# Kernel tuning notes

Measured on AMD Instinct MI355X. Metric: run time of the kernel, lower is better.

The kernel has to match this reference:

```python
import jax, jax.numpy as jnp
import numpy as np

DIM, E, K, H = 1024, 8, 2, 4096

def setup_inputs() -> dict:
    key = jax.random.key(0)
    ks = jax.random.split(key, 5)
    s_in = 1.0 / np.sqrt(DIM)
    s_h = 1.0 / np.sqrt(H)
    return {
        "x": jax.random.normal(ks[0], (4, 2048, DIM), dtype=jnp.float32),
        "Wr": jax.random.normal(ks[1], (DIM, E), dtype=jnp.float32) * s_in,
        "W1": jax.random.normal(ks[2], (E, DIM, H), dtype=jnp.float32) * s_in,
        "b1": jnp.zeros((E, H), dtype=jnp.float32),
        "W2": jax.random.normal(ks[3], (E, H, DIM), dtype=jnp.float32) * s_h,
        "b2": jnp.zeros((E, DIM), dtype=jnp.float32),
    }

def reference(x, Wr, W1, b1, W2, b2):
    batch, seq, dim = x.shape
    x_flat = x.reshape(-1, dim)                      # [T, D]
    logits = x_flat @ Wr                             # [T, E]
    w, ind = jax.lax.top_k(logits, K)                # [T, K]
    w = jax.nn.softmax(w, axis=-1)
    # combine[t, e] = sum_i w[t, i] * (ind[t, i] == e)
    combine = jnp.einsum('tke,tk->te', jax.nn.one_hot(ind, E, dtype=x.dtype), w)  # [T, E]

    def body(acc, params):
        W1e, b1e, W2e, b2e, ce = params
        h = jax.nn.gelu(x_flat @ W1e + b1e, approximate=False)  # exact GELU (torch nn.GELU default)
        y = h @ W2e + b2e                                        # [T, D]
        return acc + ce[:, None] * y, None

    out0 = jnp.zeros_like(x_flat)
    out, _ = jax.lax.scan(body, out0, (W1, b1, W2, b2, combine.T))
    return out.reshape(batch, seq, dim)
```

## Files before the change

### kernel.cpp

```cpp
#include <hip/hip_runtime.h>
#include <hip/hip_bf16.h>

#define TDIM 1024
#define NEXP 8
#define NHID 4096

typedef __hip_bfloat16 bf16;
typedef __attribute__((ext_vector_type(8))) short bf16x8;
typedef __attribute__((ext_vector_type(8))) unsigned short u16x8;
typedef __attribute__((ext_vector_type(4))) float f32x4;

__device__ __forceinline__ void gload_lds16(void* lds, const void* g) {
  __builtin_amdgcn_global_load_lds(
      (const __attribute__((address_space(1))) unsigned int*)g,
      (__attribute__((address_space(3))) unsigned int*)lds, 16, 0, 0);
}

__device__ __forceinline__ unsigned short f2bf_bits(float f) {
  __hip_bfloat16 b = __float2bfloat16(f);
  unsigned short u;
  __builtin_memcpy(&u, &b, 2);
  return u;
}

__device__ __forceinline__ float bf2f(unsigned short u) {
  union { unsigned int i; float f; } c;
  c.i = ((unsigned int)u) << 16;
  return c.f;
}

__global__ void cvt_x_kernel(const float* __restrict__ x, bf16* __restrict__ xb, int n4) {
  int i = blockIdx.x * blockDim.x + threadIdx.x;
  if (i >= n4) return;
  float4 v = reinterpret_cast<const float4*>(x)[i];
  ushort4 o;
  o.x = f2bf_bits(v.x);
  o.y = f2bf_bits(v.y);
  o.z = f2bf_bits(v.z);
  o.w = f2bf_bits(v.w);
  reinterpret_cast<ushort4*>(xb)[i] = o;
}

__global__ __launch_bounds__(256) void transpose_cvt_kernel(const float* __restrict__ in,
                                                            bf16* __restrict__ out, int R, int C) {
  __shared__ float tile[64][65];
  const size_t eoff = (size_t)blockIdx.z * R * C;
  const float* src = in + eoff;
  bf16* dst = out + eoff;
  const int c0 = blockIdx.x * 64, r0 = blockIdx.y * 64;
  const int tid = threadIdx.x;
#pragma unroll
  for (int i = 0; i < 4; ++i) {
    int s = tid + i * 256;
    int r = s >> 4, cg = (s & 15) * 4;
    float4 v = *reinterpret_cast<const float4*>(src + (size_t)(r0 + r) * C + c0 + cg);
    tile[r][cg] = v.x;
    tile[r][cg + 1] = v.y;
    tile[r][cg + 2] = v.z;
    tile[r][cg + 3] = v.w;
  }
  __syncthreads();
#pragma unroll
  for (int i = 0; i < 2; ++i) {
    int s = tid + i * 256;
    int c = s >> 3, rg = (s & 7) * 8;
    u16x8 o;
#pragma unroll
    for (int j = 0; j < 8; ++j) o[j] = f2bf_bits(tile[rg + j][c]);
    *reinterpret_cast<u16x8*>(dst + (size_t)(c0 + c) * R + r0 + rg) = o;
  }
}

__global__ void router_kernel(const float* __restrict__ x, const float* __restrict__ Wr,
                              int* __restrict__ idx, float* __restrict__ wtok,
                              int* __restrict__ cnt, int T) {
  int wave = (blockIdx.x * blockDim.x + threadIdx.x) >> 6;
  int lane = threadIdx.x & 63;
  if (wave >= T) return;
  const float4* xr4 = reinterpret_cast<const float4*>(x + (size_t)wave * TDIM);
  const float4* wr4 = reinterpret_cast<const float4*>(Wr);
  float acc[NEXP];
#pragma unroll
  for (int e = 0; e < NEXP; ++e) acc[e] = 0.f;
#pragma unroll
  for (int i = 0; i < TDIM / 256; ++i) {
    float4 xv = xr4[lane + i * 64];
    int row = (lane + i * 64) * 4;
#pragma unroll
    for (int j = 0; j < 4; ++j) {
      float xs = (&xv.x)[j];
      float4 wa = wr4[(row + j) * 2];
      float4 wb = wr4[(row + j) * 2 + 1];
      acc[0] += xs * wa.x;
      acc[1] += xs * wa.y;
      acc[2] += xs * wa.z;
      acc[3] += xs * wa.w;
      acc[4] += xs * wb.x;
      acc[5] += xs * wb.y;
      acc[6] += xs * wb.z;
      acc[7] += xs * wb.w;
    }
  }
#pragma unroll
  for (int e = 0; e < NEXP; ++e) {
    float v = acc[e];
#pragma unroll
    for (int s = 32; s; s >>= 1) v += __shfl_xor(v, s);
    acc[e] = v;
  }
  if (lane == 0) {
    int e0 = 0;
    float l0 = acc[0];
    for (int e = 1; e < NEXP; ++e)
      if (acc[e] > l0) { l0 = acc[e]; e0 = e; }
    int e1 = -1;
    float l1 = -INFINITY;
    for (int e = 0; e < NEXP; ++e)
      if (e != e0 && acc[e] > l1) { l1 = acc[e]; e1 = e; }
    float z = __expf(l1 - l0);
    float w0 = 1.f / (1.f + z);
    float w1 = z / (1.f + z);
    idx[wave * 2] = e0;
    idx[wave * 2 + 1] = e1;
    wtok[wave * 2] = w0;
    wtok[wave * 2 + 1] = w1;
    atomicAdd(&cnt[e0], 1);
    atomicAdd(&cnt[e1], 1);
  }
}

__global__ void scan_kernel(const int* __restrict__ cnt, int* __restrict__ offs) {
  if (threadIdx.x == 0 && blockIdx.x == 0) {
    int s = 0;
    for (int e = 0; e < NEXP; ++e) { offs[e] = s; s += cnt[e]; }
  }
}

__global__ void build_perm_kernel(const int* __restrict__ idx, const int* __restrict__ offs,
                                  int* __restrict__ fill, int* __restrict__ perm,
                                  int* __restrict__ islot, int T) {
  int t = blockIdx.x * blockDim.x + threadIdx.x;
  if (t >= T) return;
#pragma unroll
  for (int k = 0; k < 2; ++k) {
    int e = idx[t * 2 + k];
    int p = offs[e] + atomicAdd(&fill[e], 1);
    perm[p] = t;
    islot[t * 2 + k] = p;
  }
}

template <int KD, int ND, bool GATHER, bool GELU>
__global__ __launch_bounds__(512, 2) void moe_gemm8(
    const bf16* __restrict__ A, const bf16* __restrict__ BT, const float* __restrict__ bias,
    const int* __restrict__ perm, const int* __restrict__ cnt, const int* __restrict__ offs,
    bf16* __restrict__ Dst, int nm, int nn) {
  __shared__ short lds[65536];

  const int nwg = NEXP * nm * nn;
  const int bid = blockIdx.x;
  const int wg = (bid & 7) * (nwg >> 3) + (bid >> 3);
  const int e = wg / (nm * nn);
  const int rem = wg % (nm * nn);
  const int mb = rem / nn, nb = rem % nn;

  const int ce = cnt[e];
  const int m0 = mb * 256;
  if (m0 >= ce) return;
  const int base = offs[e];
  const int n0 = nb * 256;
  const int tid = threadIdx.x;
  const int lane = tid & 63;
  const int wid = tid >> 6;
  const int wm = wid >> 2, wn = wid & 3;
  const int lcol = lane & 15;
  const int lkg = (lane >> 4) * 8;

  const int kxs0 = ((lkg << 1) ^ ((lcol & 7) << 4)) >> 1;
  const int kxs1 = (((lkg + 32) << 1) ^ ((lcol & 7) << 4)) >> 1;
  int aRow[4], bRow[2];
#pragma unroll
  for (int mm = 0; mm < 4; ++mm) aRow[mm] = (wm * 64 + mm * 16 + lcol) << 6;
#pragma unroll
  for (int n2 = 0; n2 < 2; ++n2) bRow[n2] = (wn * 32 + n2 * 16 + lcol) << 6;

  const bf16* aP[2][2];
  const bf16* bP[2][2];
#pragma unroll
  for (int h = 0; h < 2; ++h)
#pragma unroll
    for (int i = 0; i < 2; ++i) {
      int s = tid + i * 512;
      int srow = s >> 3;
      int kof = ((s & 7) ^ (srow & 7)) * 8;
      int grow = m0 + h * 128 + srow;
      if (grow > ce - 1) grow = ce - 1;
      size_t arow = GATHER ? (size_t)perm[base + grow] : (size_t)(base + grow);
      aP[h][i] = A + arow * KD + kof;
      bP[h][i] = BT + ((size_t)e * ND + n0 + h * 128 + srow) * KD + kof;
    }

  f32x4 acc[8][4];
#pragma unroll
  for (int m = 0; m < 8; ++m)
#pragma unroll
    for (int n = 0; n < 4; ++n) acc[m][n] = (f32x4){0.f, 0.f, 0.f, 0.f};

#define STAGE(SBUF, OP, HF, kof)                                                     \
  {                                                                                  \
    char* sd = (char*)lds + (SBUF) * 65536 + (OP) * 32768 + (HF) * 16384 + tid * 16; \
    gload_lds16(sd, ((OP) ? bP[HF][0] : aP[HF][0]) + (kof));                         \
    gload_lds16(sd + 8192, ((OP) ? bP[HF][1] : aP[HF][1]) + (kof));                  \
  }

#define PHASE(p, CBUF, SBUF, kof, DO_VM)                                             \
  {                                                                                  \
    constexpr int OP = (p) & 1;                           \
    constexpr int HF = ((p) >> 1) & 1;                  \
    STAGE(SBUF, OP, HF, kof);                                                        \
    if (DO_VM) asm volatile("s_waitcnt vmcnt(6)" ::: "memory");                      \
    __builtin_amdgcn_s_barrier();                                                    \
    asm volatile("" ::: "memory");                                                   \
    const short* Ab = lds + (CBUF) * 32768 + OP * 8192;                              \
    const short* Bb = lds + (CBUF) * 32768 + 16384 + HF * 8192;                      \
    bf16x8 fA[4][2], fB[2][2];                                                       \
    _Pragma("unroll") for (int n2 = 0; n2 < 2; ++n2) {                               \
      fB[n2][0] = *(const bf16x8*)(Bb + bRow[n2] + kxs0);                            \
      fB[n2][1] = *(const bf16x8*)(Bb + bRow[n2] + kxs1);                            \
    }                                                                                \
    _Pragma("unroll") for (int mm = 0; mm < 4; ++mm) {                               \
      fA[mm][0] = *(const bf16x8*)(Ab + aRow[mm] + kxs0);                            \
      fA[mm][1] = *(const bf16x8*)(Ab + aRow[mm] + kxs1);                            \
    }                                                                                \
    asm volatile("s_waitcnt lgkmcnt(0)" ::: "memory");                               \
    __builtin_amdgcn_s_setprio(1);                                                   \
    _Pragma("unroll") for (int mm = 0; mm < 4; ++mm)                                 \
        _Pragma("unroll") for (int n2 = 0; n2 < 2; ++n2) {                           \
      acc[OP * 4 + mm][HF * 2 + n2] = __builtin_amdgcn_mfma_f32_16x16x32_bf16(       \
          fA[mm][0], fB[n2][0], acc[OP * 4 + mm][HF * 2 + n2], 0, 0, 0);             \
      acc[OP * 4 + mm][HF * 2 + n2] = __builtin_amdgcn_mfma_f32_16x16x32_bf16(       \
          fA[mm][1], fB[n2][1], acc[OP * 4 + mm][HF * 2 + n2], 0, 0, 0);             \
    }                                                                                \
    __builtin_amdgcn_s_setprio(0);                                                   \
  }

  STAGE(0, 0, 0, 0);
  STAGE(0, 1, 0, 0);
  STAGE(0, 0, 1, 0);
  STAGE(0, 1, 1, 0);

  const int NI = KD / 128;
  for (int itv = 0; itv < NI; ++itv) {
    const int k1 = itv * 128 + 64;
    int k2 = itv * 128 + 128;
    if (k2 >= KD) k2 = 0;
    PHASE(0, 0, 1, k1, 1)
    PHASE(1, 0, 1, k1, 1)
    PHASE(2, 0, 1, k1, 1)
    PHASE(3, 0, 1, k1, 0)
    PHASE(4, 1, 0, k2, 1)
    PHASE(5, 1, 0, k2, 1)
    PHASE(6, 1, 0, k2, 1)
    PHASE(7, 1, 0, k2, 0)
  }
#undef PHASE
#undef STAGE

  float bv[4];
#pragma unroll
  for (int ni = 0; ni < 4; ++ni)
    bv[ni] = bias[e * ND + n0 + (ni >> 1) * 128 + wn * 32 + (ni & 1) * 16 + lcol];
  const int lr4 = (lane >> 4) * 4;
#pragma unroll
  for (int mi = 0; mi < 8; ++mi) {
    const int rbase = m0 + (mi >> 2) * 128 + wm * 64 + (mi & 3) * 16 + lr4;
#pragma unroll
    for (int r = 0; r < 4; ++r) {
      int grow = rbase + r;
      if (grow < ce) {
        bf16* drow = Dst + (size_t)(base + grow) * ND;
#pragma unroll
        for (int ni = 0; ni < 4; ++ni) {
          int col = n0 + (ni >> 1) * 128 + wn * 32 + (ni & 1) * 16 + lcol;
          float v = acc[mi][ni][r] + bv[ni];
          if (GELU) v = 0.5f * v * (1.0f + erff(v * 0.70710678118654752f));
          drow[col] = __float2bfloat16(v);
        }
      }
    }
  }
}

__global__ void combine_kernel(const bf16* __restrict__ y, const int* __restrict__ islot,
                               const float* __restrict__ wtok, float* __restrict__ out) {
  const int t = blockIdx.x;
  const int d = threadIdx.x * 4;
  const int s0 = islot[t * 2], s1 = islot[t * 2 + 1];
  const float w0 = wtok[t * 2], w1 = wtok[t * 2 + 1];
  ushort4 ya = *reinterpret_cast<const ushort4*>(y + (size_t)s0 * TDIM + d);
  ushort4 yb = *reinterpret_cast<const ushort4*>(y + (size_t)s1 * TDIM + d);
  float4 o;
  o.x = w0 * bf2f(ya.x) + w1 * bf2f(yb.x);
  o.y = w0 * bf2f(ya.y) + w1 * bf2f(yb.y);
  o.z = w0 * bf2f(ya.z) + w1 * bf2f(yb.z);
  o.w = w0 * bf2f(ya.w) + w1 * bf2f(yb.w);
  *reinterpret_cast<float4*>(out + (size_t)t * TDIM + d) = o;
}

extern "C" void kernel_launch(void* const* d_in, const int* in_sizes, int n_in, void* d_out,
                              int out_size, void* d_ws, size_t ws_size, hipStream_t stream) {
  const float* x = (const float*)d_in[0];
  const float* Wr = (const float*)d_in[1];
  const float* W1 = (const float*)d_in[2];
  const float* b1 = (const float*)d_in[3];
  const float* W2 = (const float*)d_in[4];
  const float* b2 = (const float*)d_in[5];
  float* out = (float*)d_out;
  const int T = in_sizes[0] / TDIM;

  size_t off = 0;
  auto alloc = [&](size_t bytes) {
    void* q = (char*)d_ws + off;
    off += (bytes + 255) & ~(size_t)255;
    return q;
  };
  bf16* xb = (bf16*)alloc((size_t)T * TDIM * 2);
  bf16* W1T = (bf16*)alloc((size_t)NEXP * TDIM * NHID * 2);
  bf16* W2T = (bf16*)alloc((size_t)NEXP * TDIM * NHID * 2);
  bf16* h = (bf16*)alloc((size_t)2 * T * NHID * 2);
  int* idx = (int*)alloc((size_t)T * 2 * 4);
  float* wtok = (float*)alloc((size_t)T * 2 * 4);
  int* perm = (int*)alloc((size_t)T * 2 * 4);
  int* islot = (int*)alloc((size_t)T * 2 * 4);
  int* cnt = (int*)alloc(256);
  int* fill = cnt + 8;
  int* offs = cnt + 16;
  bf16* y = W1T;

  hipMemsetAsync(cnt, 0, 64, stream);

  cvt_x_kernel<<<(T * TDIM / 4 + 255) / 256, 256, 0, stream>>>(x, xb, T * TDIM / 4);
  transpose_cvt_kernel<<<dim3(NHID / 64, TDIM / 64, NEXP), 256, 0, stream>>>(W1, W1T, TDIM, NHID);
  transpose_cvt_kernel<<<dim3(TDIM / 64, NHID / 64, NEXP), 256, 0, stream>>>(W2, W2T, NHID, TDIM);
  router_kernel<<<T / 4, 256, 0, stream>>>(x, Wr, idx, wtok, cnt, T);
  scan_kernel<<<1, 64, 0, stream>>>(cnt, offs);
  build_perm_kernel<<<(T + 255) / 256, 256, 0, stream>>>(idx, offs, fill, perm, islot, T);

  moe_gemm8<TDIM, NHID, true, true><<<NEXP * 32 * 16, 512, 0, stream>>>(
      xb, W1T, b1, perm, cnt, offs, h, 32, 16);
  moe_gemm8<NHID, TDIM, false, false><<<NEXP * 32 * 4, 512, 0, stream>>>(
      h, W2T, b2, perm, cnt, offs, y, 32, 4);

  combine_kernel<<<T, 256, 0, stream>>>(y, islot, wtok, out);
}
```

Measured before the change: 826.7 us.

## Fuse prep kernels into one launch and reorder GEMM phases for fragment reuse

Merges the x conversion, both weight transpose-converts and the router into a single prep kernel, with the router wave also writing the bf16 copy of x so x is read once. Inside the MoE GEMM, the phase order is changed to a serpentine walk over the 2x2 quadrants so each phase reloads only the A or only the B fragments from LDS, keeping the other in registers. This cuts launch overhead, one pass over x, and half of the LDS fragment reads per phase, at the cost of longer live ranges for the fragment registers.

```diff
diff --git a/kernel.cpp b/kernel.cpp
--- a/kernel.cpp
+++ b/kernel.cpp
@@ -29,26 +29,10 @@
   return c.f;
 }
 
-__global__ void cvt_x_kernel(const float* __restrict__ x, bf16* __restrict__ xb, int n4) {
-  int i = blockIdx.x * blockDim.x + threadIdx.x;
-  if (i >= n4) return;
-  float4 v = reinterpret_cast<const float4*>(x)[i];
-  ushort4 o;
-  o.x = f2bf_bits(v.x);
-  o.y = f2bf_bits(v.y);
-  o.z = f2bf_bits(v.z);
-  o.w = f2bf_bits(v.w);
-  reinterpret_cast<ushort4*>(xb)[i] = o;
-}
-
-__global__ __launch_bounds__(256) void transpose_cvt_kernel(const float* __restrict__ in,
-                                                            bf16* __restrict__ out, int R, int C) {
-  __shared__ float tile[64][65];
-  const size_t eoff = (size_t)blockIdx.z * R * C;
-  const float* src = in + eoff;
-  bf16* dst = out + eoff;
-  const int c0 = blockIdx.x * 64, r0 = blockIdx.y * 64;
-  const int tid = threadIdx.x;
+__device__ __forceinline__ void do_transpose(const float* __restrict__ src, bf16* __restrict__ dst,
+                                             int R, int C, int bx, int by, int tid,
+                                             float (*tile)[65]) {
+  const int c0 = bx * 64, r0 = by * 64;
 #pragma unroll
   for (int i = 0; i < 4; ++i) {
     int s = tid + i * 256;
@@ -71,61 +55,83 @@
   }
 }
 
-__global__ void router_kernel(const float* __restrict__ x, const float* __restrict__ Wr,
-                              int* __restrict__ idx, float* __restrict__ wtok,
-                              int* __restrict__ cnt, int T) {
-  int wave = (blockIdx.x * blockDim.x + threadIdx.x) >> 6;
-  int lane = threadIdx.x & 63;
-  if (wave >= T) return;
-  const float4* xr4 = reinterpret_cast<const float4*>(x + (size_t)wave * TDIM);
-  const float4* wr4 = reinterpret_cast<const float4*>(Wr);
-  float acc[NEXP];
-#pragma unroll
-  for (int e = 0; e < NEXP; ++e) acc[e] = 0.f;
-#pragma unroll
-  for (int i = 0; i < TDIM / 256; ++i) {
-    float4 xv = xr4[lane + i * 64];
-    int row = (lane + i * 64) * 4;
-#pragma unroll
-    for (int j = 0; j < 4; ++j) {
-      float xs = (&xv.x)[j];
-      float4 wa = wr4[(row + j) * 2];
-      float4 wb = wr4[(row + j) * 2 + 1];
-      acc[0] += xs * wa.x;
-      acc[1] += xs * wa.y;
-      acc[2] += xs * wa.z;
-      acc[3] += xs * wa.w;
-      acc[4] += xs * wb.x;
-      acc[5] += xs * wb.y;
-      acc[6] += xs * wb.z;
-      acc[7] += xs * wb.w;
-    }
-  }
-#pragma unroll
-  for (int e = 0; e < NEXP; ++e) {
-    float v = acc[e];
-#pragma unroll
-    for (int s = 32; s; s >>= 1) v += __shfl_xor(v, s);
-    acc[e] = v;
-  }
-  if (lane == 0) {
-    int e0 = 0;
-    float l0 = acc[0];
-    for (int e = 1; e < NEXP; ++e)
-      if (acc[e] > l0) { l0 = acc[e]; e0 = e; }
-    int e1 = -1;
-    float l1 = -INFINITY;
-    for (int e = 0; e < NEXP; ++e)
-      if (e != e0 && acc[e] > l1) { l1 = acc[e]; e1 = e; }
-    float z = __expf(l1 - l0);
-    float w0 = 1.f / (1.f + z);
-    float w1 = z / (1.f + z);
-    idx[wave * 2] = e0;
-    idx[wave * 2 + 1] = e1;
-    wtok[wave * 2] = w0;
-    wtok[wave * 2 + 1] = w1;
-    atomicAdd(&cnt[e0], 1);
-    atomicAdd(&cnt[e1], 1);
+__global__ __launch_bounds__(256) void prep_kernel(
+    const float* __restrict__ W1, bf16* __restrict__ W1T, const float* __restrict__ W2,
+    bf16* __restrict__ W2T, const float* __restrict__ x, bf16* __restrict__ xb,
+    const float* __restrict__ Wr, int* __restrict__ idx, float* __restrict__ wtok,
+    int* __restrict__ cnt, int T) {
+  __shared__ float tile[64][65];
+  const int pb = blockIdx.x;
+  const int tid = threadIdx.x;
+  if (pb < 8192) {
+    const int bx = pb & 63, by = (pb >> 6) & 15, e = pb >> 10;
+    do_transpose(W1 + (size_t)e * TDIM * NHID, W1T + (size_t)e * TDIM * NHID, TDIM, NHID, bx, by,
+                 tid, tile);
+  } else if (pb < 16384) {
+    const int p = pb - 8192;
+    const int bx = p & 15, by = (p >> 4) & 63, e = p >> 10;
+    do_transpose(W2 + (size_t)e * TDIM * NHID, W2T + (size_t)e * TDIM * NHID, NHID, TDIM, bx, by,
+                 tid, tile);
+  } else {
+    const int p = pb - 16384;
+    const int wave = p * 4 + (tid >> 6);
+    const int lane = tid & 63;
+    if (wave >= T) return;
+    const float4* xr4 = reinterpret_cast<const float4*>(x + (size_t)wave * TDIM);
+    bf16* xbrow = xb + (size_t)wave * TDIM;
+    float acc[NEXP];
+#pragma unroll
+    for (int e = 0; e < NEXP; ++e) acc[e] = 0.f;
+    const float4* wr4 = reinterpret_cast<const float4*>(Wr);
+#pragma unroll
+    for (int i = 0; i < TDIM / 256; ++i) {
+      float4 xv = xr4[lane + i * 64];
+      ushort4 o;
+      o.x = f2bf_bits(xv.x);
+      o.y = f2bf_bits(xv.y);
+      o.z = f2bf_bits(xv.z);
+      o.w = f2bf_bits(xv.w);
+      *reinterpret_cast<ushort4*>(xbrow + (lane + i * 64) * 4) = o;
+      int row = (lane + i * 64) * 4;
+#pragma unroll
+      for (int j = 0; j < 4; ++j) {
+        float xs = (&xv.x)[j];
+        float4 wa = wr4[(row + j) * 2];
+        float4 wb = wr4[(row + j) * 2 + 1];
+        acc[0] += xs * wa.x;
+        acc[1] += xs * wa.y;
+        acc[2] += xs * wa.z;
+        acc[3] += xs * wa.w;
+        acc[4] += xs * wb.x;
+        acc[5] += xs * wb.y;
+        acc[6] += xs * wb.z;
+        acc[7] += xs * wb.w;
+      }
+    }
+#pragma unroll
+    for (int e = 0; e < NEXP; ++e) {
+      float v = acc[e];
+#pragma unroll
+      for (int s = 32; s; s >>= 1) v += __shfl_xor(v, s);
+      acc[e] = v;
+    }
+    if (lane == 0) {
+      int e0 = 0;
+      float l0 = acc[0];
+      for (int e = 1; e < NEXP; ++e)
+        if (acc[e] > l0) { l0 = acc[e]; e0 = e; }
+      int e1 = -1;
+      float l1 = -INFINITY;
+      for (int e = 0; e < NEXP; ++e)
+        if (e != e0 && acc[e] > l1) { l1 = acc[e]; e1 = e; }
+      float z = __expf(l1 - l0);
+      idx[wave * 2] = e0;
+      idx[wave * 2 + 1] = e1;
+      wtok[wave * 2] = 1.f / (1.f + z);
+      wtok[wave * 2 + 1] = z / (1.f + z);
+      atomicAdd(&cnt[e0], 1);
+      atomicAdd(&cnt[e1], 1);
+    }
   }
 }
 
@@ -206,6 +212,8 @@
 #pragma unroll
     for (int n = 0; n < 4; ++n) acc[m][n] = (f32x4){0.f, 0.f, 0.f, 0.f};
 
+  bf16x8 fA[4][2], fB[2][2];
+
 #define STAGE(SBUF, OP, HF, kof)                                                     \
   {                                                                                  \
     char* sd = (char*)lds + (SBUF) * 65536 + (OP) * 32768 + (HF) * 16384 + tid * 16; \
@@ -213,33 +221,34 @@
     gload_lds16(sd + 8192, ((OP) ? bP[HF][1] : aP[HF][1]) + (kof));                  \
   }
 
-#define PHASE(p, CBUF, SBUF, kof, DO_VM)                                             \
+#define PHASE(QM, QN, RA, RB, SOP, SHF, SBUF, CBUF, kof, DO_VM)                      \
   {                                                                                  \
-    constexpr int OP = (p) & 1;                           \
-    constexpr int HF = ((p) >> 1) & 1;                  \
-    STAGE(SBUF, OP, HF, kof);                                                        \
+    STAGE(SBUF, SOP, SHF, kof);                                                      \
     if (DO_VM) asm volatile("s_waitcnt vmcnt(6)" ::: "memory");                      \
     __builtin_amdgcn_s_barrier();                                                    \
     asm volatile("" ::: "memory");                                                   \
-    const short* Ab = lds + (CBUF) * 32768 + OP * 8192;                              \
-    const short* Bb = lds + (CBUF) * 32768 + 16384 + HF * 8192;                      \
-    bf16x8 fA[4][2], fB[2][2];                                                       \
-    _Pragma("unroll") for (int n2 = 0; n2 < 2; ++n2) {                               \
-      fB[n2][0] = *(const bf16x8*)(Bb + bRow[n2] + kxs0);                            \
-      fB[n2][1] = *(const bf16x8*)(Bb + bRow[n2] + kxs1);                            \
+    if (RA) {                                                                        \
+      const short* Ab = lds + (CBUF) * 32768 + (QM) * 8192;                          \
+      _Pragma("unroll") for (int mm = 0; mm < 4; ++mm) {                             \
+        fA[mm][0] = *(const bf16x8*)(Ab + aRow[mm] + kxs0);                          \
+        fA[mm][1] = *(const bf16x8*)(Ab + aRow[mm] + kxs1);                          \
+      }                                                                              \
     }                                                                                \
-    _Pragma("unroll") for (int mm = 0; mm < 4; ++mm) {                               \
-      fA[mm][0] = *(const bf16x8*)(Ab + aRow[mm] + kxs0);                            \
-      fA[mm][1] = *(const bf16x8*)(Ab + aRow[mm] + kxs1);                            \
+    if (RB) {                                                                        \
+      const short* Bb = lds + (CBUF) * 32768 + 16384 + (QN) * 8192;                  \
+      _Pragma("unroll") for (int n2 = 0; n2 < 2; ++n2) {                             \
+        fB[n2][0] = *(const bf16x8*)(Bb + bRow[n2] + kxs0);                          \
+        fB[n2][1] = *(const bf16x8*)(Bb + bRow[n2] + kxs1);                          \
+      }                                                                              \
     }                                                                                \
     asm volatile("s_waitcnt lgkmcnt(0)" ::: "memory");                               \
     __builtin_amdgcn_s_setprio(1);                                                   \
     _Pragma("unroll") for (int mm = 0; mm < 4; ++mm)                                 \
         _Pragma("unroll") for (int n2 = 0; n2 < 2; ++n2) {                           \
-      acc[OP * 4 + mm][HF * 2 + n2] = __builtin_amdgcn_mfma_f32_16x16x32_bf16(       \
-          fA[mm][0], fB[n2][0], acc[OP * 4 + mm][HF * 2 + n2], 0, 0, 0);             \
-      acc[OP * 4 + mm][HF * 2 + n2] = __builtin_amdgcn_mfma_f32_16x16x32_bf16(       \
-          fA[mm][1], fB[n2][1], acc[OP * 4 + mm][HF * 2 + n2], 0, 0, 0);             \
+      acc[(QM) * 4 + mm][(QN) * 2 + n2] = __builtin_amdgcn_mfma_f32_16x16x32_bf16(   \
+          fA[mm][0], fB[n2][0], acc[(QM) * 4 + mm][(QN) * 2 + n2], 0, 0, 0);         \
+      acc[(QM) * 4 + mm][(QN) * 2 + n2] = __builtin_amdgcn_mfma_f32_16x16x32_bf16(   \
+          fA[mm][1], fB[n2][1], acc[(QM) * 4 + mm][(QN) * 2 + n2], 0, 0, 0);         \
     }                                                                                \
     __builtin_amdgcn_s_setprio(0);                                                   \
   }
@@ -254,14 +263,14 @@
     const int k1 = itv * 128 + 64;
     int k2 = itv * 128 + 128;
     if (k2 >= KD) k2 = 0;
-    PHASE(0, 0, 1, k1, 1)
-    PHASE(1, 0, 1, k1, 1)
-    PHASE(2, 0, 1, k1, 1)
-    PHASE(3, 0, 1, k1, 0)
-    PHASE(4, 1, 0, k2, 1)
-    PHASE(5, 1, 0, k2, 1)
-    PHASE(6, 1, 0, k2, 1)
-    PHASE(7, 1, 0, k2, 0)
+    PHASE(0, 0, 1, 1, 0, 0, 1, 0, k1, 1)
+    PHASE(1, 0, 1, 0, 1, 0, 1, 0, k1, 1)
+    PHASE(1, 1, 0, 1, 0, 1, 1, 0, k1, 1)
+    PHASE(0, 1, 1, 0, 1, 1, 1, 0, k1, 0)
+    PHASE(0, 0, 1, 1, 0, 0, 0, 1, k2, 1)
+    PHASE(1, 0, 1, 0, 1, 0, 0, 1, k2, 1)
+    PHASE(1, 1, 0, 1, 0, 1, 0, 1, k2, 1)
+    PHASE(0, 1, 1, 0, 1, 1, 0, 1, k2, 0)
   }
 #undef PHASE
 #undef STAGE
@@ -339,10 +348,7 @@
 
   hipMemsetAsync(cnt, 0, 64, stream);
 
-  cvt_x_kernel<<<(T * TDIM / 4 + 255) / 256, 256, 0, stream>>>(x, xb, T * TDIM / 4);
-  transpose_cvt_kernel<<<dim3(NHID / 64, TDIM / 64, NEXP), 256, 0, stream>>>(W1, W1T, TDIM, NHID);
-  transpose_cvt_kernel<<<dim3(TDIM / 64, NHID / 64, NEXP), 256, 0, stream>>>(W2, W2T, NHID, TDIM);
-  router_kernel<<<T / 4, 256, 0, stream>>>(x, Wr, idx, wtok, cnt, T);
+  prep_kernel<<<18432, 256, 0, stream>>>(W1, W1T, W2, W2T, x, xb, Wr, idx, wtok, cnt, T);
   scan_kernel<<<1, 64, 0, stream>>>(cnt, offs);
   build_perm_kernel<<<(T + 255) / 256, 256, 0, stream>>>(idx, offs, fill, perm, islot, T);
 
```

New measurement: 782.6 us. 1.06x faster.
